# Performance work log

Hardware: AMD Instinct MI355X
Metric: run time of the kernel (lower is better)

Reference implementation:

```python
import jax, jax.numpy as jnp
import numpy as np
from jax import lax

EMBED = 64
FRAMES = 3
NNB = FRAMES - 1  # neighbor frames


def conv3x3(x, w, b):
    # x: [B,Cin,H,W], w: [Cout,Cin,3,3]
    y = lax.conv_general_dilated(x, w, (1, 1), [(1, 1), (1, 1)],
                                 dimension_numbers=("NCHW", "OIHW", "NCHW"))
    return y + b[None, :, None, None]


def setup_inputs() -> dict:
    key = jax.random.key(0)
    ks = jax.random.split(key, 9)
    s = lambda *sh: 1.0 / np.sqrt(np.prod(sh[1:]))
    return {
        "neighbor_frames": jax.random.normal(ks[0], (2, NNB, 96, 96), jnp.float32),
        "enc_w1": jax.random.normal(ks[1], (EMBED, 1, 3, 3), jnp.float32) * s(EMBED, 1, 3, 3),
        "enc_b1": jnp.zeros((EMBED,), jnp.float32),
        "enc_w2": jax.random.normal(ks[2], (EMBED, EMBED, 3, 3), jnp.float32) * s(EMBED, EMBED, 3, 3),
        "enc_b2": jnp.zeros((EMBED,), jnp.float32),
        "q_w": jax.random.normal(ks[3], (EMBED, NNB * EMBED), jnp.float32) * s(EMBED, NNB * EMBED),
        "q_b": jnp.zeros((EMBED,), jnp.float32),
        "k_w": jax.random.normal(ks[4], (EMBED, NNB * EMBED), jnp.float32) * s(EMBED, NNB * EMBED),
        "k_b": jnp.zeros((EMBED,), jnp.float32),
        "v_w": jax.random.normal(ks[5], (EMBED, NNB * EMBED), jnp.float32) * s(EMBED, NNB * EMBED),
        "v_b": jnp.zeros((EMBED,), jnp.float32),
    }


def reference(neighbor_frames, enc_w1, enc_b1, enc_w2, enc_b2,
              q_w, q_b, k_w, k_b, v_w, v_b):
    B, N, H, W = neighbor_frames.shape
    x = neighbor_frames.reshape(B * N, 1, H, W)
    # conv encoder (3x3 -> relu -> 3x3 -> relu)
    f = jax.nn.relu(conv3x3(x, enc_w1, enc_b1))
    f = jax.nn.relu(conv3x3(f, enc_w2, enc_b2))
    C = f.shape[1]
    # [B,N,C,H,W] -> [B, C*N? no: permute(0,2,1,3,4) -> B, C, N, H, W -> B, C*N, H, W]
    feat = f.reshape(B, N, C, H, W).transpose(0, 2, 1, 3, 4).reshape(B, C * N, H, W)
    # 1x1 qkv convs == per-pixel linear; flatten spatial to tokens t = H*W
    feat_t = feat.reshape(B, C * N, H * W)  # [B, Cin, T]
    Q = jnp.einsum("oc,bct->bot", q_w, feat_t) + q_b[None, :, None]
    K = jnp.einsum("oc,bct->bot", k_w, feat_t) + k_b[None, :, None]
    V = jnp.einsum("oc,bct->bot", v_w, feat_t) + v_b[None, :, None]
    scale = 1.0 / jnp.sqrt(jnp.asarray(Q.shape[1], Q.dtype))
    attn = jnp.einsum("bcn,bcm->bnm", Q, K) * scale  # [B, T, T]
    attn = jax.nn.softmax(attn, axis=-1)
    ctx = jnp.einsum("bnm,bcm->bcn", attn, V)  # [B, C, T]
    return ctx.reshape(B, C, H, W)
```

## Files before the change

kernel.cpp:

```cpp
#include <hip/hip_runtime.h>
#include <hip/hip_bf16.h>

#define TOK 9216
#define KSPLIT 5

typedef _Float16 half8 __attribute__((ext_vector_type(8)));
typedef float f32x4 __attribute__((ext_vector_type(4)));

#define GLOAD_LDS(g, l) \
    __builtin_amdgcn_global_load_lds((const __attribute__((address_space(1))) void*)(g), \
                                     (__attribute__((address_space(3))) void*)(l), 16, 0, 0)

#define QSCALE 0.18033688011112042f

#define OFF_F1   0u
#define SZ_F1    (4u*64u*TOK)
#define OFF_FEAT (OFF_F1 + SZ_F1)
#define SZ_FEAT  (2u*128u*TOK)
#define OFF_Q    (OFF_FEAT + SZ_FEAT)
#define SZ_QKV   (2u*64u*TOK)
#define OFF_K    (OFF_Q + SZ_QKV)
#define OFF_V    (OFF_K + SZ_QKV)
#define OFF_W1   (OFF_V + SZ_QKV)
#define OFF_B1   (OFF_W1 + 576u)
#define OFF_W2T  (OFF_B1 + 64u)
#define OFF_B2   (OFF_W2T + 36864u)
#define OFF_WCAT (OFF_B2 + 64u)
#define OFF_BCAT (OFF_WCAT + 24576u)

#define OFF_QT   OFF_F1
#define OFF_KT   (OFF_F1 + 589824u)
#define OFF_VH   (OFF_F1 + 1179648u)

#define OFF_SLAB0 1769472u
#define OFF_ML2   (OFF_FEAT + 9u*589824u)

__device__ __forceinline__ const float* part_base_c(const float* ws, int slab) {
    return ws + (slab == 0 ? OFF_SLAB0 : (OFF_FEAT + (unsigned)(slab - 1) * 589824u));
}
__device__ __forceinline__ float* part_base(float* ws, int slab) {
    return ws + (slab == 0 ? OFF_SLAB0 : (OFF_FEAT + (unsigned)(slab - 1) * 589824u));
}

__global__ __launch_bounds__(256) void prep_kernel(
    const float* __restrict__ w1, const float* __restrict__ b1,
    const float* __restrict__ w2, const float* __restrict__ b2,
    const float* __restrict__ qw, const float* __restrict__ qb,
    const float* __restrict__ kw, const float* __restrict__ kb,
    const float* __restrict__ vw, const float* __restrict__ vb,
    float* __restrict__ ws)
{
    int gid = blockIdx.x * 256 + threadIdx.x;
    if (gid < 576) ws[OFF_W1 + gid] = w1[gid];
    if (gid < 64) {
        ws[OFF_B1 + gid] = b1[gid];
        ws[OFF_B2 + gid] = b2[gid];
    }
    if (gid < 36864) {
        int co = gid / 576; int rem = gid % 576;
        int ci = rem / 9;  int tp = rem % 9;
        ((_Float16*)(ws + OFF_W2T))[co*576 + tp*64 + ci] = (_Float16)w2[gid];
    }
    if (gid < 24576) {
        int o = gid >> 7; int kidx = gid & 127;
        int n = kidx >> 6, c = kidx & 63;
        int sc = c*2 + n;
        float v;
        if (o < 64)       v = qw[o*128 + sc] * QSCALE;
        else if (o < 128) v = kw[(o-64)*128 + sc];
        else              v = vw[(o-128)*128 + sc];
        ((_Float16*)(ws + OFF_WCAT))[gid] = (_Float16)v;
    }
    if (gid < 192) {
        float v;
        if (gid < 64)       v = qb[gid] * QSCALE;
        else if (gid < 128) v = kb[gid-64];
        else                v = vb[gid-128];
        ws[OFF_BCAT + gid] = v;
    }
}

__global__ __launch_bounds__(256) void conv1_kernel(
    const float* __restrict__ x, float* __restrict__ ws)
{
    const float* w1f = ws + OFF_W1;
    const float* b1f = ws + OFF_B1;
    _Float16* f1h = (_Float16*)(ws + OFF_F1);
    int gid = blockIdx.x * 256 + threadIdx.x;
    int img = gid / TOK;
    int p   = gid % TOK;
    int h = p / 96, w = p % 96;
    float xv[9];
    #pragma unroll
    for (int dh = 0; dh < 3; ++dh)
        #pragma unroll
        for (int dw = 0; dw < 3; ++dw) {
            int r = h + dh - 1, c = w + dw - 1;
            bool ok = (r >= 0) && (r < 96) && (c >= 0) && (c < 96);
            xv[dh*3 + dw] = ok ? x[img*TOK + r*96 + c] : 0.f;
        }
    _Float16* dst = f1h + (size_t)gid * 64;
    #pragma unroll
    for (int g8 = 0; g8 < 8; ++g8) {
        union { _Float16 h[8]; uint4 u; } pk8;
        #pragma unroll
        for (int j = 0; j < 8; ++j) {
            int co = g8*8 + j;
            float a = b1f[co];
            #pragma unroll
            for (int t = 0; t < 9; ++t) a += w1f[co*9 + t] * xv[t];
            pk8.h[j] = (_Float16)fmaxf(a, 0.f);
        }
        *(uint4*)&dst[g8*8] = pk8.u;
    }
}

__global__ __launch_bounds__(256) void conv2_kernel(float* __restrict__ ws)
{
    int bid = blockIdx.x;
    int img = bid & 3;
    int tile = bid >> 2;
    int tid = threadIdx.x;
    int lane = tid & 63, w = tid >> 6;
    int lr = lane & 15, lk = lane >> 4;

    const _Float16* f1h = (const _Float16*)(ws + OFF_F1) + (size_t)img*TOK*64;
    const _Float16* Wc  = (const _Float16*)(ws + OFF_W2T);
    const float* b2f = ws + OFF_B2;

    int t = tile*64 + w*16 + lr;
    int h = t / 96, wc = t % 96;

    half8 z8;
    #pragma unroll
    for (int i = 0; i < 8; ++i) z8[i] = (_Float16)0.f;

    f32x4 acc[4];
    #pragma unroll
    for (int cs = 0; cs < 4; ++cs) {
        float bv = b2f[cs*16 + lr];
        acc[cs] = (f32x4){bv, bv, bv, bv};
    }

    #pragma unroll
    for (int ch = 0; ch < 18; ++ch) {
        int k = ch*32 + lk*8;
        int tap = k >> 6, ci = k & 63;
        int dh = tap / 3, dw = tap % 3;
        int r = h + dh - 1, c = wc + dw - 1;
        half8 af = z8;
        if ((unsigned)r < 96u && (unsigned)c < 96u)
            af = *(const half8*)&f1h[(size_t)(r*96 + c)*64 + ci];
        #pragma unroll
        for (int cs = 0; cs < 4; ++cs) {
            half8 bfr = *(const half8*)&Wc[(size_t)(cs*16 + lr)*576 + k];
            acc[cs] = __builtin_amdgcn_mfma_f32_16x16x32_f16(af, bfr, acc[cs], 0, 0, 0);
        }
    }

    _Float16* featH2 = (_Float16*)(ws + OFF_FEAT) + (size_t)img*TOK*64;
    int tbase = tile*64 + w*16 + 4*lk;
    #pragma unroll
    for (int cs = 0; cs < 4; ++cs)
        #pragma unroll
        for (int r = 0; r < 4; ++r)
            featH2[(size_t)(tbase + r)*64 + cs*16 + lr] = (_Float16)fmaxf(acc[cs][r], 0.f);
}

__global__ __launch_bounds__(256) void qkvgemm_kernel(float* __restrict__ ws)
{
    int bid = blockIdx.x;
    int b   = bid / 288;
    int tt0 = (bid % 288) * 32;
    int tid = threadIdx.x;
    int lane = tid & 63, w = tid >> 6;
    int lr = lane & 15, lk = lane >> 4;

    const _Float16* fH = (const _Float16*)(ws + OFF_FEAT) + (size_t)b*2*TOK*64;
    const _Float16* W  = (const _Float16*)(ws + OFF_WCAT);
    const float* bc = ws + OFF_BCAT;
    _Float16* QT = (_Float16*)(ws + OFF_QT) + (size_t)b*TOK*64;
    _Float16* KT = (_Float16*)(ws + OFF_KT) + (size_t)b*TOK*64;
    _Float16* VH = (_Float16*)(ws + OFF_VH) + (size_t)b*64*TOK;

    half8 bf[2][4];
    #pragma unroll
    for (int tt = 0; tt < 2; ++tt)
        #pragma unroll
        for (int kc = 0; kc < 4; ++kc) {
            int k = kc*32 + lk*8;
            bf[tt][kc] = *(const half8*)&fH[(size_t)(k >> 6)*TOK*64
                                            + (size_t)(tt0 + tt*16 + lr)*64 + (k & 63)];
        }

    half8 af[3][4];
    #pragma unroll
    for (int i = 0; i < 3; ++i)
        #pragma unroll
        for (int kc = 0; kc < 4; ++kc)
            af[i][kc] = *(const half8*)&W[(size_t)((w*3 + i)*16 + lr)*128 + kc*32 + lk*8];

    #pragma unroll
    for (int i = 0; i < 3; ++i) {
        int ot = w*3 + i;
        f32x4 a0, a1;
        #pragma unroll
        for (int r = 0; r < 4; ++r) {
            float bv = bc[ot*16 + 4*lk + r];
            a0[r] = bv; a1[r] = bv;
        }
        #pragma unroll
        for (int kc = 0; kc < 4; ++kc) {
            a0 = __builtin_amdgcn_mfma_f32_16x16x32_f16(af[i][kc], bf[0][kc], a0, 0, 0, 0);
            a1 = __builtin_amdgcn_mfma_f32_16x16x32_f16(af[i][kc], bf[1][kc], a1, 0, 0, 0);
        }
        #pragma unroll
        for (int tt = 0; tt < 2; ++tt) {
            f32x4 a = tt ? a1 : a0;
            int t = tt0 + tt*16 + lr;
            if (ot < 4) {
                union { _Float16 h[4]; uint2 u; } p;
                #pragma unroll
                for (int r = 0; r < 4; ++r) p.h[r] = (_Float16)a[r];
                *(uint2*)&QT[(size_t)t*64 + ot*16 + 4*lk] = p.u;
            } else if (ot < 8) {
                union { _Float16 h[4]; uint2 u; } p;
                #pragma unroll
                for (int r = 0; r < 4; ++r) p.h[r] = (_Float16)a[r];
                *(uint2*)&KT[(size_t)t*64 + (ot-4)*16 + 4*lk] = p.u;
            } else {
                #pragma unroll
                for (int r = 0; r < 4; ++r)
                    VH[(size_t)((ot-8)*16 + 4*lk + r)*TOK + t] = (_Float16)a[r];
            }
        }
    }
}

__global__ __launch_bounds__(256, 5) void attn_kernel(float* __restrict__ ws)
{
    __shared__ __align__(16) char smem[32768];
    float* ldsf = (float*)smem;

    int bid = blockIdx.x;
    int b   = bid / (144*KSPLIT);
    int rem = bid % (144*KSPLIT);
    int qt  = rem / KSPLIT;
    int ks  = rem % KSPLIT;
    int tid = threadIdx.x;
    int lane = tid & 63, w = tid >> 6;
    int q0 = qt * 64;
    int lr = lane & 15;
    int lk = lane >> 4;

    int kb0 = (ks*144)/KSPLIT, kb1 = ((ks+1)*144)/KSPLIT;
    int nit = kb1 - kb0;
    int slab = b*KSPLIT + ks;

    const _Float16* Qt = (const _Float16*)(ws + OFF_QT) + (size_t)b*TOK*64;
    const _Float16* Kt = (const _Float16*)(ws + OFF_KT) + (size_t)b*TOK*64;
    const _Float16* Vh = (const _Float16*)(ws + OFF_VH) + (size_t)b*64*TOK;
    float* part = part_base(ws, slab);
    float* ml   = ws + OFF_ML2 + (size_t)slab*2*TOK;

    half8 qB[2];
    #pragma unroll
    for (int ch = 0; ch < 2; ++ch)
        qB[ch] = *(const half8*)&Qt[(size_t)(q0 + w*16 + lr)*64 + ch*32 + lk*8];

    const f32x4 Z4 = (f32x4){0.f, 0.f, 0.f, 0.f};
    half8 ones;
    #pragma unroll
    for (int i = 0; i < 8; ++i) ones[i] = (_Float16)1.0f;

    f32x4 O[4];
    #pragma unroll
    for (int cs = 0; cs < 4; ++cs) O[cs] = Z4;
    f32x4 lacc = Z4;
    float mM = -INFINITY;

    int segl = ((lane & 7) ^ ((lane >> 3) & 7)) * 8;
    unsigned rbase = (unsigned)(w*16 + (lane >> 3));
    unsigned kOff = (unsigned)(kb0*64 + rbase)*64u + (unsigned)segl;
    unsigned vOff = rbase*(unsigned)TOK + (unsigned)(kb0*64) + (unsigned)segl;
    unsigned wk0 = (unsigned)(w * 2048);

    {
        char* bK = smem;
        char* bV = smem + 8192;
        GLOAD_LDS(Kt + kOff,           bK + wk0);
        GLOAD_LDS(Kt + kOff + 512,     bK + wk0 + 1024);
        GLOAD_LDS(Vh + vOff,           bV + wk0);
        GLOAD_LDS(Vh + vOff + 8u*TOK,  bV + wk0 + 1024);
    }
    asm volatile("s_waitcnt vmcnt(0)" ::: "memory");
    __builtin_amdgcn_s_barrier();

    for (int it = 0; it < nit; ++it) {
        char* sKb = smem + (it & 1) * 16384;
        char* sVb = sKb + 8192;
        char* sSt = smem + ((it + 1) & 1) * 16384;

        if (it + 1 < nit) {
            unsigned kN = kOff + (unsigned)(it + 1) * 4096u;
            unsigned vN = vOff + (unsigned)(it + 1) * 64u;
            GLOAD_LDS(Kt + kN,           sSt + wk0);
            GLOAD_LDS(Kt + kN + 512,     sSt + wk0 + 1024);
            GLOAD_LDS(Vh + vN,           sSt + 8192 + wk0);
            GLOAD_LDS(Vh + vN + 8u*TOK,  sSt + 8192 + wk0 + 1024);
        }

        f32x4 S[4];
        __builtin_amdgcn_s_setprio(1);
        #pragma unroll
        for (int st = 0; st < 4; ++st) {
            int t = st*16 + lr;
            half8 kA0 = *(const half8*)(sKb + ((t*128 +       lk*16) ^ ((t&7)<<4)));
            half8 kA1 = *(const half8*)(sKb + ((t*128 + 64 +  lk*16) ^ ((t&7)<<4)));
            f32x4 s = __builtin_amdgcn_mfma_f32_16x16x32_f16(kA0, qB[0], Z4, 0, 0, 0);
            S[st]   = __builtin_amdgcn_mfma_f32_16x16x32_f16(kA1, qB[1], s,  0, 0, 0);
        }
        __builtin_amdgcn_s_setprio(0);

        float a0 = fmaxf(fmaxf(S[0][0], S[0][1]), S[0][2]);
        float a1 = fmaxf(fmaxf(S[0][3], S[1][0]), S[1][1]);
        float a2 = fmaxf(fmaxf(S[1][2], S[1][3]), S[2][0]);
        float a3 = fmaxf(fmaxf(S[2][1], S[2][2]), S[2][3]);
        float a4 = fmaxf(fmaxf(S[3][0], S[3][1]), S[3][2]);
        float pm = fmaxf(fmaxf(fmaxf(a0, a1), a2),
                         fmaxf(fmaxf(a3, a4), S[3][3]));
        pm = fmaxf(pm, __shfl_xor(pm, 16));
        pm = fmaxf(pm, __shfl_xor(pm, 32));

        if (__any(pm > mM + 8.0f)) {
            float mn = fmaxf(mM, pm);
            float fs = exp2f(mM - mn);
            mM = mn;
            #pragma unroll
            for (int cs = 0; cs < 4; ++cs)
                #pragma unroll
                for (int r = 0; r < 4; ++r) O[cs][r] *= fs;
            #pragma unroll
            for (int r = 0; r < 4; ++r) lacc[r] *= fs;
        }

        #pragma unroll
        for (int st = 0; st < 4; ++st)
            #pragma unroll
            for (int r = 0; r < 4; ++r)
                S[st][r] = exp2f(S[st][r] - mM);

        unsigned int pk[4][2];
        #pragma unroll
        for (int st = 0; st < 4; ++st) {
            union { _Float16 h[2]; unsigned int u; } c0, c1;
            c0.h[0] = (_Float16)S[st][0]; c0.h[1] = (_Float16)S[st][1];
            c1.h[0] = (_Float16)S[st][2]; c1.h[1] = (_Float16)S[st][3];
            pk[st][0] = c0.u; pk[st][1] = c1.u;
        }

        int srcA = lr + 32*(lk & 1);
        int sel  = lk >> 1;
        __builtin_amdgcn_s_setprio(1);
        #pragma unroll
        for (int ch2 = 0; ch2 < 2; ++ch2) {
            union { unsigned int u[4]; half8 h; } pb;
            #pragma unroll
            for (int w2 = 0; w2 < 4; ++w2) {
                int src = srcA + 16*(w2 >> 1);
                int lo = __shfl((int)pk[ch2*2 + 0][w2 & 1], src);
                int hi = __shfl((int)pk[ch2*2 + 1][w2 & 1], src);
                pb.u[w2] = (unsigned int)(sel ? hi : lo);
            }
            lacc = __builtin_amdgcn_mfma_f32_16x16x32_f16(ones, pb.h, lacc, 0, 0, 0);
            #pragma unroll
            for (int cs = 0; cs < 4; ++cs) {
                int crow = cs*16 + lr;
                half8 vA = *(const half8*)(sVb + ((crow*128 + ch2*64 + lk*16) ^ ((crow&7)<<4)));
                O[cs] = __builtin_amdgcn_mfma_f32_16x16x32_f16(vA, pb.h, O[cs], 0, 0, 0);
            }
        }
        __builtin_amdgcn_s_setprio(0);

        asm volatile("s_waitcnt vmcnt(0)" ::: "memory");
        __builtin_amdgcn_s_barrier();
    }

    if (lk == 0) {
        ml[q0 + w*16 + lr]       = mM;
        ml[TOK + q0 + w*16 + lr] = lacc[0];
    }

    #pragma unroll
    for (int cs = 0; cs < 4; ++cs)
        #pragma unroll
        for (int r = 0; r < 4; ++r)
            ldsf[(cs*16 + 4*lk + r)*68 + w*16 + lr] = O[cs][r];
    __syncthreads();
    int c = tid >> 2, sg = tid & 3;
    const float* srcr = &ldsf[c*68 + sg*16];
    float* dstr = &part[(size_t)c*TOK + q0 + sg*16];
    #pragma unroll
    for (int j = 0; j < 4; ++j)
        *(float4*)&dstr[j*4] = *(const float4*)&srcr[j*4];
}

__global__ __launch_bounds__(256) void recombine_kernel(
    const float* __restrict__ ws, float* __restrict__ out)
{
    int gid = blockIdx.x * 256 + threadIdx.x;
    int b   = gid / (4*TOK);
    int rem = gid % (4*TOK);
    int cg  = rem / TOK;
    int t   = rem % TOK;
    const float* mlp = ws + OFF_ML2;

    float m[KSPLIT], l[KSPLIT];
    float M = -INFINITY;
    #pragma unroll
    for (int ks = 0; ks < KSPLIT; ++ks) {
        int slab = b*KSPLIT + ks;
        m[ks] = mlp[(size_t)slab*2*TOK + t];
        l[ks] = mlp[(size_t)slab*2*TOK + TOK + t];
        M = fmaxf(M, m[ks]);
    }
    float wgt[KSPLIT];
    float denom = 0.f;
    #pragma unroll
    for (int ks = 0; ks < KSPLIT; ++ks) {
        wgt[ks] = exp2f(m[ks] - M);
        denom += l[ks] * wgt[ks];
    }
    float inv = 1.f / denom;
    #pragma unroll
    for (int cc = 0; cc < 16; ++cc) {
        int c = cg*16 + cc;
        float acc = 0.f;
        #pragma unroll
        for (int ks = 0; ks < KSPLIT; ++ks) {
            const float* part = part_base_c(ws, b*KSPLIT + ks);
            acc += part[(size_t)c*TOK + t] * wgt[ks];
        }
        out[(size_t)(b*64 + c)*TOK + t] = acc * inv;
    }
}

extern "C" void kernel_launch(void* const* d_in, const int* in_sizes, int n_in,
                              void* d_out, int out_size, void* d_ws, size_t ws_size,
                              hipStream_t stream)
{
    const float* frames = (const float*)d_in[0];
    const float* w1 = (const float*)d_in[1];
    const float* b1 = (const float*)d_in[2];
    const float* w2 = (const float*)d_in[3];
    const float* b2 = (const float*)d_in[4];
    const float* qw = (const float*)d_in[5];
    const float* qb = (const float*)d_in[6];
    const float* kw = (const float*)d_in[7];
    const float* kb = (const float*)d_in[8];
    const float* vw = (const float*)d_in[9];
    const float* vb = (const float*)d_in[10];
    float* ws = (float*)d_ws;
    float* out = (float*)d_out;

    hipLaunchKernelGGL(prep_kernel, dim3(144), dim3(256), 0, stream,
                       w1, b1, w2, b2, qw, qb, kw, kb, vw, vb, ws);
    hipLaunchKernelGGL(conv1_kernel, dim3(144), dim3(256), 0, stream, frames, ws);
    hipLaunchKernelGGL(conv2_kernel, dim3(576), dim3(256), 0, stream, ws);
    hipLaunchKernelGGL(qkvgemm_kernel, dim3(576), dim3(256), 0, stream, ws);
    hipLaunchKernelGGL(attn_kernel, dim3(2*144*KSPLIT), dim3(256), 0, stream, ws);
    hipLaunchKernelGGL(recombine_kernel, dim3(288), dim3(256), 0, stream, ws, out);
}
```

Baseline: 175.6 us.

## Halve attention key tile to 32 and shrink LDS to raise occupancy

The attention kernel now processes 32 keys per iteration instead of 64, and the double-buffered K/V staging shrinks from 32 KB to about 17 KB of LDS. Launch bounds go from 5 to 8 blocks per SIMD group, with a new V swizzle and one global-to-LDS load per buffer. The fp16 packing of probabilities now uses cvt_pkrtz. This aims to hide latency through higher occupancy, at the cost of twice as many loop iterations and barriers and more per-iteration softmax overhead. Round-toward-zero conversion also slightly changes numerics.

New measurement: 174.3 us. Within noise of the previous version (-0.7%).

```diff
diff --git a/kernel.cpp b/kernel.cpp
--- a/kernel.cpp
+++ b/kernel.cpp
@@ -237,9 +237,9 @@
     }
 }
 
-__global__ __launch_bounds__(256, 5) void attn_kernel(float* __restrict__ ws)
-{
-    __shared__ __align__(16) char smem[32768];
+__global__ __launch_bounds__(256, 8) void attn_kernel(float* __restrict__ ws)
+{
+    __shared__ __align__(16) char smem[17408];
     float* ldsf = (float*)smem;
 
     int bid = blockIdx.x;
@@ -253,7 +253,7 @@
     int lr = lane & 15;
     int lk = lane >> 4;
 
-    int kb0 = (ks*144)/KSPLIT, kb1 = ((ks+1)*144)/KSPLIT;
+    int kb0 = (ks*288)/KSPLIT, kb1 = ((ks+1)*288)/KSPLIT;
     int nit = kb1 - kb0;
     int slab = b*KSPLIT + ks;
 
@@ -279,56 +279,44 @@
     f32x4 lacc = Z4;
     float mM = -INFINITY;
 
-    int segl = ((lane & 7) ^ ((lane >> 3) & 7)) * 8;
-    unsigned rbase = (unsigned)(w*16 + (lane >> 3));
-    unsigned kOff = (unsigned)(kb0*64 + rbase)*64u + (unsigned)segl;
-    unsigned vOff = rbase*(unsigned)TOK + (unsigned)(kb0*64) + (unsigned)segl;
-    unsigned wk0 = (unsigned)(w * 2048);
-
-    {
-        char* bK = smem;
-        char* bV = smem + 8192;
-        GLOAD_LDS(Kt + kOff,           bK + wk0);
-        GLOAD_LDS(Kt + kOff + 512,     bK + wk0 + 1024);
-        GLOAD_LDS(Vh + vOff,           bV + wk0);
-        GLOAD_LDS(Vh + vOff + 8u*TOK,  bV + wk0 + 1024);
-    }
+    int ksegl = ((lane & 7) ^ ((lane >> 3) & 7)) * 8;
+    int vsegl = ((lane & 3) ^ ((lane >> 2) & 3)) * 8;
+    unsigned kOff = (unsigned)(kb0*32 + w*8 + (lane >> 3))*64u + (unsigned)ksegl;
+    unsigned vOff = (unsigned)(w*16 + (lane >> 2))*(unsigned)TOK
+                    + (unsigned)(kb0*32) + (unsigned)vsegl;
+    unsigned wbase = (unsigned)(w * 1024);
+
+    GLOAD_LDS(Kt + kOff, smem +        wbase);
+    GLOAD_LDS(Vh + vOff, smem + 8192 + wbase);
     asm volatile("s_waitcnt vmcnt(0)" ::: "memory");
     __builtin_amdgcn_s_barrier();
 
     for (int it = 0; it < nit; ++it) {
-        char* sKb = smem + (it & 1) * 16384;
-        char* sVb = sKb + 8192;
-        char* sSt = smem + ((it + 1) & 1) * 16384;
+        char* sKb = smem +        (it & 1) * 4096;
+        char* sVb = smem + 8192 + (it & 1) * 4096;
 
         if (it + 1 < nit) {
-            unsigned kN = kOff + (unsigned)(it + 1) * 4096u;
-            unsigned vN = vOff + (unsigned)(it + 1) * 64u;
-            GLOAD_LDS(Kt + kN,           sSt + wk0);
-            GLOAD_LDS(Kt + kN + 512,     sSt + wk0 + 1024);
-            GLOAD_LDS(Vh + vN,           sSt + 8192 + wk0);
-            GLOAD_LDS(Vh + vN + 8u*TOK,  sSt + 8192 + wk0 + 1024);
-        }
-
-        f32x4 S[4];
+            unsigned kN = kOff + (unsigned)(it + 1) * 2048u;
+            unsigned vN = vOff + (unsigned)(it + 1) * 32u;
+            GLOAD_LDS(Kt + kN, smem +        ((it + 1) & 1) * 4096 + wbase);
+            GLOAD_LDS(Vh + vN, smem + 8192 + ((it + 1) & 1) * 4096 + wbase);
+        }
+
+        f32x4 S[2];
         __builtin_amdgcn_s_setprio(1);
         #pragma unroll
-        for (int st = 0; st < 4; ++st) {
+        for (int st = 0; st < 2; ++st) {
             int t = st*16 + lr;
-            half8 kA0 = *(const half8*)(sKb + ((t*128 +       lk*16) ^ ((t&7)<<4)));
-            half8 kA1 = *(const half8*)(sKb + ((t*128 + 64 +  lk*16) ^ ((t&7)<<4)));
+            half8 kA0 = *(const half8*)(sKb + ((t*128 +      lk*16) ^ ((t&7)<<4)));
+            half8 kA1 = *(const half8*)(sKb + ((t*128 + 64 + lk*16) ^ ((t&7)<<4)));
             f32x4 s = __builtin_amdgcn_mfma_f32_16x16x32_f16(kA0, qB[0], Z4, 0, 0, 0);
             S[st]   = __builtin_amdgcn_mfma_f32_16x16x32_f16(kA1, qB[1], s,  0, 0, 0);
         }
         __builtin_amdgcn_s_setprio(0);
 
-        float a0 = fmaxf(fmaxf(S[0][0], S[0][1]), S[0][2]);
-        float a1 = fmaxf(fmaxf(S[0][3], S[1][0]), S[1][1]);
-        float a2 = fmaxf(fmaxf(S[1][2], S[1][3]), S[2][0]);
-        float a3 = fmaxf(fmaxf(S[2][1], S[2][2]), S[2][3]);
-        float a4 = fmaxf(fmaxf(S[3][0], S[3][1]), S[3][2]);
-        float pm = fmaxf(fmaxf(fmaxf(a0, a1), a2),
-                         fmaxf(fmaxf(a3, a4), S[3][3]));
+        float m0 = fmaxf(fmaxf(S[0][0], S[0][1]), fmaxf(S[0][2], S[0][3]));
+        float m1 = fmaxf(fmaxf(S[1][0], S[1][1]), fmaxf(S[1][2], S[1][3]));
+        float pm = fmaxf(m0, m1);
         pm = fmaxf(pm, __shfl_xor(pm, 16));
         pm = fmaxf(pm, __shfl_xor(pm, 32));
 
@@ -345,40 +333,38 @@
         }
 
         #pragma unroll
-        for (int st = 0; st < 4; ++st)
+        for (int st = 0; st < 2; ++st)
             #pragma unroll
             for (int r = 0; r < 4; ++r)
                 S[st][r] = exp2f(S[st][r] - mM);
 
-        unsigned int pk[4][2];
-        #pragma unroll
-        for (int st = 0; st < 4; ++st) {
-            union { _Float16 h[2]; unsigned int u; } c0, c1;
-            c0.h[0] = (_Float16)S[st][0]; c0.h[1] = (_Float16)S[st][1];
-            c1.h[0] = (_Float16)S[st][2]; c1.h[1] = (_Float16)S[st][3];
-            pk[st][0] = c0.u; pk[st][1] = c1.u;
+        unsigned int pk2[2][2];
+        #pragma unroll
+        for (int st = 0; st < 2; ++st) {
+            pk2[st][0] = __builtin_bit_cast(unsigned int,
+                             __builtin_amdgcn_cvt_pkrtz(S[st][0], S[st][1]));
+            pk2[st][1] = __builtin_bit_cast(unsigned int,
+                             __builtin_amdgcn_cvt_pkrtz(S[st][2], S[st][3]));
         }
 
         int srcA = lr + 32*(lk & 1);
         int sel  = lk >> 1;
+        union { unsigned int u[4]; half8 h; } pb;
+        #pragma unroll
+        for (int w2 = 0; w2 < 4; ++w2) {
+            int src = srcA + 16*(w2 >> 1);
+            int lo = __shfl((int)pk2[0][w2 & 1], src);
+            int hi = __shfl((int)pk2[1][w2 & 1], src);
+            pb.u[w2] = (unsigned int)(sel ? hi : lo);
+        }
+
         __builtin_amdgcn_s_setprio(1);
-        #pragma unroll
-        for (int ch2 = 0; ch2 < 2; ++ch2) {
-            union { unsigned int u[4]; half8 h; } pb;
-            #pragma unroll
-            for (int w2 = 0; w2 < 4; ++w2) {
-                int src = srcA + 16*(w2 >> 1);
-                int lo = __shfl((int)pk[ch2*2 + 0][w2 & 1], src);
-                int hi = __shfl((int)pk[ch2*2 + 1][w2 & 1], src);
-                pb.u[w2] = (unsigned int)(sel ? hi : lo);
-            }
-            lacc = __builtin_amdgcn_mfma_f32_16x16x32_f16(ones, pb.h, lacc, 0, 0, 0);
-            #pragma unroll
-            for (int cs = 0; cs < 4; ++cs) {
-                int crow = cs*16 + lr;
-                half8 vA = *(const half8*)(sVb + ((crow*128 + ch2*64 + lk*16) ^ ((crow&7)<<4)));
-                O[cs] = __builtin_amdgcn_mfma_f32_16x16x32_f16(vA, pb.h, O[cs], 0, 0, 0);
-            }
+        lacc = __builtin_amdgcn_mfma_f32_16x16x32_f16(ones, pb.h, lacc, 0, 0, 0);
+        #pragma unroll
+        for (int cs = 0; cs < 4; ++cs) {
+            int crow = cs*16 + lr;
+            half8 vA = *(const half8*)(sVb + ((crow*64 + lk*16) ^ ((crow&3)<<4)));
+            O[cs] = __builtin_amdgcn_mfma_f32_16x16x32_f16(vA, pb.h, O[cs], 0, 0, 0);
         }
         __builtin_amdgcn_s_setprio(0);
 
```
